# Performance work log

Measured on AMD Instinct MI355X. Metric: run time of the kernel, lower is better.

The kernel has to match this reference:

```python
import jax, jax.numpy as jnp
import numpy as np

L, N, E, F, D, ED, G = 3, 40000, 640000, 32, 64, 64, 16
EPS_LN = 1e-5
silu = jax.nn.silu


def graph_ln(x, gids, gamma, beta):
    # Per-graph LayerNorm: normalize over (nodes_in_graph, features), affine per feature.
    Dn = x.shape[1]
    cnt = jax.ops.segment_sum(jnp.ones((x.shape[0],), x.dtype), gids, num_segments=G) * Dn
    mean = jax.ops.segment_sum(x.sum(1), gids, num_segments=G) / cnt
    ex2 = jax.ops.segment_sum((x * x).sum(1), gids, num_segments=G) / cnt
    inv = jax.lax.rsqrt(ex2 - mean * mean + EPS_LN)
    return (x - mean[gids, None]) * inv[gids, None] * gamma + beta


def setup_inputs() -> dict:
    key = jax.random.key(0)
    it = iter(jax.random.split(key, 64))
    def rn(shape, s=0.1):
        return jax.random.normal(next(it), shape, jnp.float32) * s
    return {
        "node_features": jax.random.normal(next(it), (N, F), jnp.float32),
        "node_positions": jax.random.normal(next(it), (N, 3), jnp.float32) * 3.0,
        "edges": jax.random.randint(next(it), (E, 2), 0, N),
        "graph_ids": jnp.sort(jax.random.randint(next(it), (N,), 0, G)),
        "proj_W1": rn((F, F)), "proj_b1": jnp.zeros((F,), jnp.float32),
        "proj_W2": rn((F, D)), "proj_b2": jnp.zeros((D,), jnp.float32),
        "ef_W": rn((L, 1, ED)), "ef_b": jnp.zeros((L, ED), jnp.float32),
        "el_W1": rn((L, ED + 2 * D, 2 * D)), "el_b1": jnp.zeros((L, 2 * D), jnp.float32),
        "el_W2": rn((L, 2 * D, ED)), "el_b2": jnp.zeros((L, ED), jnp.float32),
        "in_W": rn((L, ED, 3 * D)), "in_b": jnp.zeros((L, 3 * D), jnp.float32),
        "msg_W1": rn((L, D, D)), "msg_b1": jnp.zeros((L, D), jnp.float32),
        "msg_W2": rn((L, D, 3 * D)), "msg_b2": jnp.zeros((L, 3 * D), jnp.float32),
        "ei_W": rn((L, D, 1)), "ei_b": jnp.zeros((L, 1), jnp.float32),
        "ln_g": jnp.ones((L, D), jnp.float32), "ln_b": jnp.zeros((L, D), jnp.float32),
        "up_UV": rn((L, D, 2 * D)),
        "uv_W1": rn((L, 2 * D, D)), "uv_b1": jnp.zeros((L, D), jnp.float32),
        "uv_W2": rn((L, D, 3 * D)), "uv_b2": jnp.zeros((L, 3 * D), jnp.float32),
    }


def _forward(node_features, node_positions, proj_W1, proj_b1, proj_W2, proj_b2,
             ef_W, ef_b, el_W1, el_b1, el_W2, el_b2, in_W, in_b,
             msg_W1, msg_b1, msg_W2, msg_b2, ei_W, ei_b, ln_g, ln_b,
             up_UV, uv_W1, uv_b1, uv_W2, uv_b2, edges, graph_ids):
    src, dst = edges[:, 0], edges[:, 1]
    diff = node_positions[dst] - node_positions[src]            # [E,3]
    dist = jnp.sqrt((diff * diff).sum(-1) + 1e-12)              # [E]
    unit = diff / dist[:, None]                                 # [E,3]
    edge_emb = dist[:, None]                                    # [E,1] (rbf_layer=None)
    s = silu(node_features @ proj_W1 + proj_b1) @ proj_W2 + proj_b2   # [N,D]
    v = jnp.zeros((s.shape[0], 3, D), s.dtype)                  # [N,3,D]
    for l in range(L):
        # edge featurizer
        es = silu(edge_emb @ ef_W[l] + ef_b[l])                 # [E,ED]
        # EdgeLayer (residual=False)
        cat = jnp.concatenate([s[src], s[dst], es], axis=1)     # [E,2D+ED]
        es = silu(cat @ el_W1[l] + el_b1[l]) @ el_W2[l] + el_b2[l]
        # InteractionLayer
        sn = graph_ln(s, graph_ids, ln_g[l], ln_b[l])
        Wv = es @ in_W[l] + in_b[l]                             # [E,3D]
        phi = silu(sn @ msg_W1[l] + msg_b1[l]) @ msg_W2[l] + msg_b2[l]  # [N,3D]
        Wphi = Wv * phi[src]
        phi_s, phi_vv, phi_vs = jnp.split(Wphi, 3, axis=1)
        gate = jax.nn.sigmoid(phi_s @ ei_W[l] + ei_b[l])        # [E,1]
        ms = phi_s * gate
        mv = (v[src] * phi_vv[:, None, :] + phi_vs[:, None, :] * unit[..., None]) * gate[:, None, :]
        s = sn + jax.ops.segment_sum(ms, dst, num_segments=N)
        v = v + jax.ops.segment_sum(mv, dst, num_segments=N)
        # UpdateLayer
        UVv = v @ up_UV[l]                                      # [N,3,2D]
        Uv, Vv = jnp.split(UVv, 2, axis=-1)
        Vv_norm = jnp.sqrt((Vv * Vv).sum(1) + 1e-6)             # [N,D]
        a = silu(jnp.concatenate([Vv_norm, s], axis=1) @ uv_W1[l] + uv_b1[l]) @ uv_W2[l] + uv_b2[l]
        a_vv, a_sv, a_ss = jnp.split(a, 3, axis=1)
        inner = (Uv * Vv).sum(1)                                # [N,D]
        s = s + a_ss + a_sv * inner
        v = v + a_vv[:, None, :] * Uv
    return s


def reference(node_features, node_positions, edges, graph_ids, proj_W1, proj_b1, proj_W2, proj_b2,
              ef_W, ef_b, el_W1, el_b1, el_W2, el_b2, in_W, in_b,
              msg_W1, msg_b1, msg_W2, msg_b2, ei_W, ei_b, ln_g, ln_b,
              up_UV, uv_W1, uv_b1, uv_W2, uv_b2):
    return _forward(node_features, node_positions, proj_W1, proj_b1, proj_W2, proj_b2,
                    ef_W, ef_b, el_W1, el_b1, el_W2, el_b2, in_W, in_b,
                    msg_W1, msg_b1, msg_W2, msg_b2, ei_W, ei_b, ln_g, ln_b,
                    up_UV, uv_W1, uv_b1, uv_W2, uv_b2, edges, graph_ids)
```

## Files before the change

kernel.cpp:

```cpp
#include <hip/hip_runtime.h>
#include <hip/hip_bf16.h>
#include <math.h>

#define NN 40000
#define EE 640000
#define GG 16
#define LL 3
#define TE 32

#define STC 200
#define STH 136
#define STE 72
#define PCAT (TE*STC)
#define PH1  (TE*STH)
#define PES  (TE*STE)
#define SWP_ST 196

typedef __attribute__((ext_vector_type(8))) short s8v;
typedef __attribute__((ext_vector_type(4))) float f4v;

__device__ __forceinline__ float silu_f(float x){ return x / (1.f + __expf(-x)); }
__device__ __forceinline__ float sigmoid_f(float x){ return 1.f / (1.f + __expf(-x)); }
__device__ __forceinline__ ushort f2b(float x){
  __hip_bfloat16 h = __float2bfloat16(x);
  return __builtin_bit_cast(ushort, h);
}
__device__ __forceinline__ float b2f(ushort u){
  uint x = ((uint)u) << 16;
  return __builtin_bit_cast(float, x);
}
__device__ __forceinline__ void split2(float v, ushort &hi, ushort &lo){
  uint b = __builtin_bit_cast(uint, v);
  hi = (ushort)(b >> 16);
  float rem = v - __builtin_bit_cast(float, b & 0xffff0000u);
  lo = (ushort)(__builtin_bit_cast(uint, rem) >> 16);
}

__global__ void k_geom(const float* __restrict__ pos, const int* __restrict__ edges,
                       float4* __restrict__ UD){
  int e = blockIdx.x*blockDim.x + threadIdx.x;
  if(e >= EE) return;
  int s = edges[2*e], d = edges[2*e+1];
  float dx = pos[3*d]-pos[3*s], dy = pos[3*d+1]-pos[3*s+1], dz = pos[3*d+2]-pos[3*s+2];
  float r = sqrtf(dx*dx+dy*dy+dz*dz + 1e-12f);
  float ir = 1.f/r;
  UD[e] = make_float4(dx*ir, dy*ir, dz*ir, r);
}

__global__ void k_counts(const int* __restrict__ gids, int* __restrict__ cnt){
  __shared__ int lb[GG+1];
  int g = threadIdx.x;
  if(g <= GG){
    int lo=0, hi=NN;
    while(lo<hi){ int m=(lo+hi)>>1; if(gids[m]<g) lo=m+1; else hi=m; }
    lb[g]=lo;
  }
  __syncthreads();
  if(g < GG) cnt[g] = lb[g+1]-lb[g];
}

__global__ void k_hist(const int* __restrict__ edges, int* __restrict__ HIST){
  int e = blockIdx.x*blockDim.x+threadIdx.x;
  if(e<EE) atomicAdd(&HIST[edges[2*e+1]], 1);
}

__global__ void k_scan(const int* __restrict__ HIST, int* __restrict__ BASE){
  __shared__ int ps[256];
  int t = threadIdx.x;
  const int CH = (NN+255)/256;
  int lo = t*CH, hi = lo+CH; if(hi>NN) hi=NN; if(lo>NN) lo=NN;
  int s=0;
  for(int i=lo;i<hi;i++) s += HIST[i];
  ps[t]=s;
  __syncthreads();
  if(t==0){ int run=0; for(int i=0;i<256;i++){ int v=ps[i]; ps[i]=run; run+=v; } }
  __syncthreads();
  int run = ps[t];
  for(int i=lo;i<hi;i++){ BASE[i]=run; run += HIST[i]; }
}

__global__ void k_scatter(const int* __restrict__ edges, const int* __restrict__ BASE,
                          int* __restrict__ CUR,
                          int* __restrict__ SRCp, int* __restrict__ DSTp,
                          const float4* __restrict__ UD, float4* __restrict__ UDP){
  int e = blockIdx.x*blockDim.x+threadIdx.x;
  if(e>=EE) return;
  int d = edges[2*e+1];
  int s = edges[2*e];
  int pos = BASE[d] + atomicAdd(&CUR[d], 1);
  SRCp[pos] = s;
  DSTp[pos] = d;
  UDP[pos]  = UD[e];
}

__global__ void k_prep_w(const float* __restrict__ elW1, const float* __restrict__ elW2,
                         const float* __restrict__ inW,
                         ushort* __restrict__ W1H, ushort* __restrict__ W1L,
                         ushort* __restrict__ W2H, ushort* __restrict__ W2L,
                         ushort* __restrict__ W3H, ushort* __restrict__ W3L){
  int tid = blockIdx.x*256 + threadIdx.x;
  const int per = 24576 + 8192 + 12288;
  if(tid >= LL*per) return;
  int l = tid/per, r = tid - l*per;
  float w; ushort* dh; ushort* dl; int idx;
  if(r < 24576){
    int n = r/192, k = r - n*192;
    w = elW1[l*24576 + k*128 + n];
    dh = W1H; dl = W1L; idx = l*24576 + r;
  } else if(r < 32768){
    int i = r - 24576; int n = i/128, k = i - n*128;
    w = elW2[l*8192 + k*64 + n];
    dh = W2H; dl = W2L; idx = l*8192 + i;
  } else {
    int i = r - 32768; int n = i/64, k = i - n*64;
    w = inW[l*12288 + k*192 + n];
    dh = W3H; dl = W3L; idx = l*12288 + i;
  }
  ushort hi = f2b(w);
  dh[idx] = hi;
  dl[idx] = f2b(w - b2f(hi));
}

__global__ void k_proj(const float* __restrict__ x,
                       const float* __restrict__ W1, const float* __restrict__ b1,
                       const float* __restrict__ W2, const float* __restrict__ b2,
                       float* __restrict__ S, ushort* __restrict__ SHL){
  int n = blockIdx.x*blockDim.x+threadIdx.x;
  if(n>=NN) return;
  float xr[32];
  #pragma unroll
  for(int k=0;k<32;k++) xr[k] = x[n*32+k];
  float h[32];
  #pragma unroll 4
  for(int j=0;j<32;j++){
    float a = b1[j];
    #pragma unroll
    for(int k=0;k<32;k++) a += xr[k]*W1[k*32+j];
    h[j] = silu_f(a);
  }
  #pragma unroll 4
  for(int d=0; d<64; d++){
    float a = b2[d];
    #pragma unroll
    for(int j=0;j<32;j++) a += h[j]*W2[j*64+d];
    S[n*64+d] = a;
    ushort hi = f2b(a);
    SHL[(size_t)n*128 + d] = hi;
    SHL[(size_t)n*128 + 64 + d] = f2b(a - b2f(hi));
  }
}

__global__ void k_ln_reduce(const float* __restrict__ S, const int* __restrict__ gids,
                            float* __restrict__ GS, float* __restrict__ GQ){
  __shared__ float ls[GG], lq[GG];
  int t = threadIdx.x;
  if(t<GG){ ls[t]=0.f; lq[t]=0.f; }
  __syncthreads();
  int n = blockIdx.x*blockDim.x+t;
  if(n<NN){
    const float4* p = reinterpret_cast<const float4*>(S + (size_t)n*64);
    float sm=0.f, sq=0.f;
    #pragma unroll
    for(int i=0;i<16;i++){ float4 v=p[i];
      sm += v.x+v.y+v.z+v.w;
      sq += v.x*v.x+v.y*v.y+v.z*v.z+v.w*v.w; }
    int g = gids[n];
    atomicAdd(&ls[g], sm); atomicAdd(&lq[g], sq);
  }
  __syncthreads();
  if(t<GG){ atomicAdd(&GS[t], ls[t]); atomicAdd(&GQ[t], lq[t]); }
}

__global__ void k_ln_final(const float* __restrict__ GS, const float* __restrict__ GQ,
                           const int* __restrict__ cnt,
                           float* __restrict__ MEANV, float* __restrict__ INVV){
  int g = threadIdx.x;
  if(g<GG){
    float c = (float)cnt[g]*64.f;
    float m = GS[g]/c, e2 = GQ[g]/c;
    MEANV[g]=m; INVV[g]=rsqrtf(e2 - m*m + 1e-5f);
  }
}

__global__ void k_node_pre(const float* __restrict__ S, const int* __restrict__ gids,
                           const float* __restrict__ MEANV, const float* __restrict__ INVV,
                           const float* __restrict__ lng, const float* __restrict__ lnb,
                           const float* __restrict__ W1, const float* __restrict__ b1,
                           const float* __restrict__ W2, const float* __restrict__ b2,
                           float* __restrict__ SN, ushort* __restrict__ PHI2){
  int t = threadIdx.x, w = t>>6, lane = t&63;
  int n = blockIdx.x*4 + w;
  __shared__ float sh[4][65];
  __shared__ float hh[4][65];
  if(n < NN){
    int g = gids[n];
    float snv = (S[(size_t)n*64+lane] - MEANV[g]) * INVV[g] * lng[lane] + lnb[lane];
    SN[(size_t)n*64+lane] = snv;
    sh[w][lane] = snv;
  }
  __syncthreads();
  if(n < NN){
    float a = b1[lane];
    #pragma unroll 8
    for(int k=0;k<64;k++) a += sh[w][k]*W1[k*64+lane];
    hh[w][lane] = silu_f(a);
  }
  __syncthreads();
  if(n < NN){
    #pragma unroll
    for(int m=0;m<3;m++){
      int j = lane + 64*m;
      float a = b2[j];
      #pragma unroll 8
      for(int k=0;k<64;k++) a += hh[w][k]*W2[k*192+j];
      ushort h_, l_; split2(a, h_, l_);
      PHI2[(size_t)n*384 + 2*j]     = h_;
      PHI2[(size_t)n*384 + 2*j + 1] = l_;
    }
  }
}

__global__ __launch_bounds__(256,3) void k_edge(
    const ushort* __restrict__ SHL, const ushort* __restrict__ PHI2,
    const ushort* __restrict__ V0b, const float4* __restrict__ UDP,
    const int* __restrict__ SRCp, const int* __restrict__ DSTp,
    const float* __restrict__ efW, const float* __restrict__ efb,
    const ushort* __restrict__ GW1H, const ushort* __restrict__ GW1L, const float* __restrict__ elb1,
    const ushort* __restrict__ GW2H, const ushort* __restrict__ GW2L, const float* __restrict__ elb2,
    const ushort* __restrict__ GW3H, const ushort* __restrict__ GW3L, const float* __restrict__ inb,
    const float* __restrict__ eiW, const float* __restrict__ eib,
    float* __restrict__ SN, float* __restrict__ V1, int hasV0)
{
  __shared__ __align__(16) ushort sCat[2*PCAT];
  __shared__ __align__(16) ushort sH1 [2*PH1];
  __shared__ __align__(16) ushort sEs [2*PES];
  __shared__ int   sSrc[TE], sDst[TE];
  __shared__ float sUnit[TE*3];
  __shared__ float sGate[TE];

  const int t  = threadIdx.x;
  const int cpx = gridDim.x >> 3;
  const int bid = (blockIdx.x & 7)*cpx + (blockIdx.x >> 3);
  const int p0 = bid * TE;
  const int w  = t >> 6, l = t & 63;
  const int lr = l & 15, lg = l >> 4;

  if(t < TE){
    int p = p0 + t;
    sSrc[t] = SRCp[p]; sDst[t] = DSTp[p];
    float4 ud = UDP[p];
    sUnit[3*t] = ud.x; sUnit[3*t+1] = ud.y; sUnit[3*t+2] = ud.z;
  }
  {
    int e = t >> 3, s = t & 7;
    int pg = p0 + e;
    int src = SRCp[pg], dst = DSTp[pg];
    float dist = UDP[pg].w;
    *reinterpret_cast<s8v*>(&sCat[e*STC + s*8]) =
        *reinterpret_cast<const s8v*>(&SHL[(size_t)src*128 + s*8]);
    *reinterpret_cast<s8v*>(&sCat[PCAT + e*STC + s*8]) =
        *reinterpret_cast<const s8v*>(&SHL[(size_t)src*128 + 64 + s*8]);
    *reinterpret_cast<s8v*>(&sCat[e*STC + 64 + s*8]) =
        *reinterpret_cast<const s8v*>(&SHL[(size_t)dst*128 + s*8]);
    *reinterpret_cast<s8v*>(&sCat[PCAT + e*STC + 64 + s*8]) =
        *reinterpret_cast<const s8v*>(&SHL[(size_t)dst*128 + 64 + s*8]);
    #pragma unroll
    for(int jj=0;jj<8;jj++){
      int j = s*8 + jj;
      float v = silu_f(dist*efW[j] + efb[j]);
      ushort h_, l_; split2(v, h_, l_);
      sCat[e*STC + 128 + j] = h_;
      sCat[PCAT + e*STC + 128 + j] = l_;
    }
  }
  __syncthreads();

  uint phu[2][3][4];
  #pragma unroll
  for(int rt=0; rt<2; rt++){
    #pragma unroll
    for(int r=0;r<4;r++){
      int srcp = sSrc[16*rt + lg*4 + r];
      #pragma unroll
      for(int jl=0;jl<3;jl++){
        int n = 16*(3*w+jl) + lr;
        phu[rt][jl][r] = *reinterpret_cast<const uint*>(&PHI2[(size_t)srcp*384 + 2*n]);
      }
    }
  }
  ushort v0pre[TE];
  if(w > 0 && hasV0){
    int c = w-1;
    #pragma unroll
    for(int p=0;p<TE;p++)
      v0pre[p] = V0b[(size_t)sSrc[p]*192 + c*64 + l];
  }

  #pragma unroll
  for(int jl=0;jl<2;jl++){
    s8v bh[6], bl[6];
    #pragma unroll
    for(int k=0;k<6;k++){
      int o = (16*(2*w+jl)+lr)*192 + k*32 + lg*8;
      bh[k] = *reinterpret_cast<const s8v*>(&GW1H[o]);
      bl[k] = *reinterpret_cast<const s8v*>(&GW1L[o]);
    }
    #pragma unroll
    for(int rt=0; rt<2; rt++){
      s8v ah[6], al[6];
      #pragma unroll
      for(int k=0;k<6;k++){
        int ro = (16*rt+lr)*STC + k*32 + lg*8;
        ah[k] = *reinterpret_cast<const s8v*>(&sCat[ro]);
        al[k] = *reinterpret_cast<const s8v*>(&sCat[PCAT + ro]);
      }
      float bv = elb1[16*(2*w+jl)+lr];
      f4v acc = (f4v){bv,bv,bv,bv};
      #pragma unroll
      for(int k=0;k<6;k++){
        acc = __builtin_amdgcn_mfma_f32_16x16x32_bf16(ah[k], bh[k], acc, 0,0,0);
        acc = __builtin_amdgcn_mfma_f32_16x16x32_bf16(al[k], bh[k], acc, 0,0,0);
        acc = __builtin_amdgcn_mfma_f32_16x16x32_bf16(ah[k], bl[k], acc, 0,0,0);
      }
      #pragma unroll
      for(int r=0;r<4;r++){
        float v = silu_f(acc[r]);
        ushort h_, l_; split2(v, h_, l_);
        int o = (16*rt + lg*4 + r)*STH + 16*(2*w+jl) + lr;
        sH1[o] = h_;
        sH1[PH1 + o] = l_;
      }
    }
  }
  __syncthreads();

  {
    s8v bh[4], bl[4];
    #pragma unroll
    for(int k=0;k<4;k++){
      int o = (16*w+lr)*128 + k*32 + lg*8;
      bh[k] = *reinterpret_cast<const s8v*>(&GW2H[o]);
      bl[k] = *reinterpret_cast<const s8v*>(&GW2L[o]);
    }
    #pragma unroll
    for(int rt=0; rt<2; rt++){
      s8v a2h[4], a2l[4];
      #pragma unroll
      for(int k=0;k<4;k++){
        int ro = (16*rt+lr)*STH + k*32 + lg*8;
        a2h[k] = *reinterpret_cast<const s8v*>(&sH1[ro]);
        a2l[k] = *reinterpret_cast<const s8v*>(&sH1[PH1 + ro]);
      }
      float bv = elb2[16*w + lr];
      f4v acc = (f4v){bv,bv,bv,bv};
      #pragma unroll
      for(int k=0;k<4;k++){
        acc = __builtin_amdgcn_mfma_f32_16x16x32_bf16(a2h[k], bh[k], acc, 0,0,0);
        acc = __builtin_amdgcn_mfma_f32_16x16x32_bf16(a2l[k], bh[k], acc, 0,0,0);
        acc = __builtin_amdgcn_mfma_f32_16x16x32_bf16(a2h[k], bl[k], acc, 0,0,0);
      }
      #pragma unroll
      for(int r=0;r<4;r++){
        ushort h_, l_; split2(acc[r], h_, l_);
        int o = (16*rt + lg*4 + r)*STE + 16*w + lr;
        sEs[o] = h_;
        sEs[PES + o] = l_;
      }
    }
  }
  __syncthreads();

  float* sWp = reinterpret_cast<float*>(sCat);
  #pragma unroll
  for(int jl=0;jl<3;jl++){
    const int n = 16*(3*w+jl) + lr;
    s8v bh[2], bl[2];
    #pragma unroll
    for(int k=0;k<2;k++){
      bh[k] = *reinterpret_cast<const s8v*>(&GW3H[n*64 + k*32 + lg*8]);
      bl[k] = *reinterpret_cast<const s8v*>(&GW3L[n*64 + k*32 + lg*8]);
    }
    #pragma unroll
    for(int rt=0; rt<2; rt++){
      s8v a3h[2], a3l[2];
      #pragma unroll
      for(int k=0;k<2;k++){
        int ro = (16*rt+lr)*STE + k*32 + lg*8;
        a3h[k] = *reinterpret_cast<const s8v*>(&sEs[ro]);
        a3l[k] = *reinterpret_cast<const s8v*>(&sEs[PES + ro]);
      }
      float bv = inb[n];
      f4v acc = (f4v){bv,bv,bv,bv};
      #pragma unroll
      for(int k=0;k<2;k++){
        acc = __builtin_amdgcn_mfma_f32_16x16x32_bf16(a3h[k], bh[k], acc, 0,0,0);
        acc = __builtin_amdgcn_mfma_f32_16x16x32_bf16(a3l[k], bh[k], acc, 0,0,0);
        acc = __builtin_amdgcn_mfma_f32_16x16x32_bf16(a3h[k], bl[k], acc, 0,0,0);
      }
      #pragma unroll
      for(int r=0;r<4;r++){
        uint u = phu[rt][jl][r];
        float phi = b2f((ushort)(u & 0xffffu)) + b2f((ushort)(u >> 16));
        sWp[(16*rt + lg*4 + r)*SWP_ST + n] = acc[r]*phi;
      }
    }
  }
  __syncthreads();

  float ei = eiW[l];
  #pragma unroll
  for(int i=0;i<8;i++){
    int e = w*8 + i;
    float gp = sWp[e*SWP_ST + l] * ei;
    #pragma unroll
    for(int off=1; off<64; off<<=1) gp += __shfl_xor(gp, off);
    if(l==0) sGate[e] = sigmoid_f(gp + eib[0]);
  }
  __syncthreads();

  if(w == 0){
    float acc = 0.f;
    #pragma unroll
    for(int p=0;p<TE;p++){
      acc += sWp[p*SWP_ST + l] * sGate[p];
      bool flush = (p==TE-1) || (sDst[p+1] != sDst[p]);
      if(flush){ atomicAdd(&SN[(size_t)sDst[p]*64 + l], acc); acc = 0.f; }
    }
  } else {
    int c = w-1;
    float acc = 0.f;
    #pragma unroll
    for(int p=0;p<TE;p++){
      float pvv = sWp[p*SWP_ST + 64 + l];
      float pvs = sWp[p*SWP_ST + 128 + l];
      float term = pvs*sUnit[p*3+c];
      if(hasV0) term += b2f(v0pre[p])*pvv;
      acc += term * sGate[p];
      bool flush = (p==TE-1) || (sDst[p+1] != sDst[p]);
      if(flush){ atomicAdd(&V1[(size_t)sDst[p]*192 + c*64 + l], acc); acc = 0.f; }
    }
  }
}

__global__ void k_node_post(const float* __restrict__ SN, const float* __restrict__ V1,
                            const float* __restrict__ upUV,
                            const float* __restrict__ uvW1, const float* __restrict__ uvb1,
                            const float* __restrict__ uvW2, const float* __restrict__ uvb2,
                            float* __restrict__ Sout, float* __restrict__ V0,
                            ushort* __restrict__ SHL, ushort* __restrict__ V0b)
{
  int t = threadIdx.x, w = t>>6, j = t&63;
  int n = blockIdx.x*4 + w;
  __shared__ float vsh[4][3][64];
  __shared__ float cat2[4][129];
  __shared__ float hh[4][65];
  if(n < NN){
    #pragma unroll
    for(int c=0;c<3;c++) vsh[w][c][j] = V1[(size_t)n*192 + c*64 + j];
  }
  __syncthreads();
  float Uv[3]={0,0,0}, Vv[3]={0,0,0};
  float s_new = 0.f;
  if(n < NN){
    #pragma unroll 4
    for(int k=0;k<64;k++){
      float wu = upUV[k*128 + j];
      float wv = upUV[k*128 + 64 + j];
      #pragma unroll
      for(int c=0;c<3;c++){ float vk = vsh[w][c][k]; Uv[c] += vk*wu; Vv[c] += vk*wv; }
    }
    s_new = SN[(size_t)n*64 + j];
    float vn2 = Vv[0]*Vv[0]+Vv[1]*Vv[1]+Vv[2]*Vv[2];
    cat2[w][j] = sqrtf(vn2 + 1e-6f);
    cat2[w][64+j] = s_new;
  }
  __syncthreads();
  if(n<NN){
    float a = uvb1[j];
    #pragma unroll 8
    for(int k=0;k<128;k++) a += cat2[w][k]*uvW1[k*64+j];
    hh[w][j] = silu_f(a);
  }
  __syncthreads();
  if(n<NN){
    float a0=uvb2[j], a1=uvb2[64+j], a2=uvb2[128+j];
    #pragma unroll 4
    for(int k=0;k<64;k++){
      float h = hh[w][k];
      a0 += h*uvW2[k*192+j]; a1 += h*uvW2[k*192+64+j]; a2 += h*uvW2[k*192+128+j];
    }
    float inner = Uv[0]*Vv[0]+Uv[1]*Vv[1]+Uv[2]*Vv[2];
    float sval = s_new + a2 + a1*inner;
    Sout[(size_t)n*64+j] = sval;
    ushort hi = f2b(sval);
    SHL[(size_t)n*128 + j] = hi;
    SHL[(size_t)n*128 + 64 + j] = f2b(sval - b2f(hi));
    #pragma unroll
    for(int c=0;c<3;c++){
      float vv = vsh[w][c][j] + a0*Uv[c];
      V0[(size_t)n*192 + c*64 + j] = vv;
      V0b[(size_t)n*192 + c*64 + j] = f2b(vv);
    }
  }
}

extern "C" void kernel_launch(void* const* d_in, const int* in_sizes, int n_in,
                              void* d_out, int out_size, void* d_ws, size_t ws_size,
                              hipStream_t stream)
{
  const float* node_features  = (const float*)d_in[0];
  const float* node_positions = (const float*)d_in[1];
  const int*   edges          = (const int*)  d_in[2];
  const int*   gids           = (const int*)  d_in[3];
  const float* proj_W1 = (const float*)d_in[4];
  const float* proj_b1 = (const float*)d_in[5];
  const float* proj_W2 = (const float*)d_in[6];
  const float* proj_b2 = (const float*)d_in[7];
  const float* ef_W  = (const float*)d_in[8];
  const float* ef_b  = (const float*)d_in[9];
  const float* el_W1 = (const float*)d_in[10];
  const float* el_b1 = (const float*)d_in[11];
  const float* el_W2 = (const float*)d_in[12];
  const float* el_b2 = (const float*)d_in[13];
  const float* in_W  = (const float*)d_in[14];
  const float* in_b  = (const float*)d_in[15];
  const float* msg_W1= (const float*)d_in[16];
  const float* msg_b1= (const float*)d_in[17];
  const float* msg_W2= (const float*)d_in[18];
  const float* msg_b2= (const float*)d_in[19];
  const float* ei_W  = (const float*)d_in[20];
  const float* ei_b  = (const float*)d_in[21];
  const float* ln_g  = (const float*)d_in[22];
  const float* ln_b  = (const float*)d_in[23];
  const float* up_UV = (const float*)d_in[24];
  const float* uv_W1 = (const float*)d_in[25];
  const float* uv_b1 = (const float*)d_in[26];
  const float* uv_W2 = (const float*)d_in[27];
  const float* uv_b2 = (const float*)d_in[28];

  float* ws = (float*)d_ws;
  size_t off = 0;
  float*  S    = ws + off; off += (size_t)NN*64;
  float*  SN   = ws + off; off += (size_t)NN*64;
  float*  V0   = ws + off; off += (size_t)NN*192;
  float*  V1   = ws + off; off += (size_t)NN*192;
  float4* UD   = (float4*)(ws + off); off += (size_t)EE*4;
  float4* UDP  = (float4*)(ws + off); off += (size_t)EE*4;
  float*  GS   = ws + off; off += GG;
  float*  GQ   = ws + off; off += GG;
  float*  MEANV= ws + off; off += GG;
  float*  INVV = ws + off; off += GG;
  int*    CNT  = (int*)(ws + off); off += GG;
  off = (off + 3) & ~(size_t)3;
  ushort* SHL  = (ushort*)(ws + off); off += (size_t)NN*64;
  ushort* PHI2 = (ushort*)(ws + off); off += (size_t)NN*192;
  ushort* V0b  = (ushort*)(ws + off); off += (size_t)NN*96;
  ushort* W1H = (ushort*)(ws + off); off += (size_t)LL*24576/2;
  ushort* W1L = (ushort*)(ws + off); off += (size_t)LL*24576/2;
  ushort* W2H = (ushort*)(ws + off); off += (size_t)LL*8192/2;
  ushort* W2L = (ushort*)(ws + off); off += (size_t)LL*8192/2;
  ushort* W3H = (ushort*)(ws + off); off += (size_t)LL*12288/2;
  ushort* W3L = (ushort*)(ws + off); off += (size_t)LL*12288/2;
  int*    HIST = (int*)(ws + off); off += NN;
  int*    BASE = (int*)(ws + off); off += NN;
  int*    CUR  = (int*)(ws + off); off += NN;
  int*    SRCp = (int*)(ws + off); off += EE;
  int*    DSTp = (int*)(ws + off); off += EE;

  hipMemsetAsync(HIST, 0, NN*sizeof(int), stream);
  hipMemsetAsync(CUR,  0, NN*sizeof(int), stream);
  hipMemsetAsync(V0, 0, (size_t)NN*192*sizeof(float), stream);
  hipMemsetAsync(V0b, 0, (size_t)NN*192*sizeof(ushort), stream);

  k_geom   <<<(EE+255)/256, 256, 0, stream>>>(node_positions, edges, UD);
  k_counts <<<1, 32, 0, stream>>>(gids, CNT);
  k_proj   <<<(NN+255)/256, 256, 0, stream>>>(node_features, proj_W1, proj_b1, proj_W2, proj_b2, S, SHL);
  k_prep_w <<<(LL*45056+255)/256, 256, 0, stream>>>(el_W1, el_W2, in_W,
                   W1H, W1L, W2H, W2L, W3H, W3L);
  k_hist   <<<(EE+255)/256, 256, 0, stream>>>(edges, HIST);
  k_scan   <<<1, 256, 0, stream>>>(HIST, BASE);
  k_scatter<<<(EE+255)/256, 256, 0, stream>>>(edges, BASE, CUR, SRCp, DSTp, UD, UDP);

  for(int l=0; l<LL; l++){
    hipMemsetAsync(GS, 0, 2*GG*sizeof(float), stream);
    k_ln_reduce<<<(NN+255)/256, 256, 0, stream>>>(S, gids, GS, GQ);
    k_ln_final <<<1, 64, 0, stream>>>(GS, GQ, CNT, MEANV, INVV);
    k_node_pre <<<(NN+3)/4, 256, 0, stream>>>(S, gids, MEANV, INVV,
                   ln_g + l*64, ln_b + l*64,
                   msg_W1 + l*64*64, msg_b1 + l*64,
                   msg_W2 + l*64*192, msg_b2 + l*192,
                   SN, PHI2);
    hipMemcpyAsync(V1, V0, (size_t)NN*192*sizeof(float), hipMemcpyDeviceToDevice, stream);
    k_edge<<<EE/TE, 256, 0, stream>>>(SHL, PHI2, V0b, UDP, SRCp, DSTp,
                   ef_W + l*64, ef_b + l*64,
                   W1H + l*24576, W1L + l*24576, el_b1 + l*128,
                   W2H + l*8192,  W2L + l*8192,  el_b2 + l*64,
                   W3H + l*12288, W3L + l*12288, in_b + l*192,
                   ei_W + l*64, ei_b + l, SN, V1, l > 0 ? 1 : 0);
    float* sout = (l == LL-1) ? (float*)d_out : S;
    k_node_post<<<(NN+3)/4, 256, 0, stream>>>(SN, V1,
                   up_UV + l*64*128,
                   uv_W1 + l*128*64, uv_b1 + l*64,
                   uv_W2 + l*64*192, uv_b2 + l*192, sout, V0, SHL, V0b);
  }
}
```

Measured before the change: 2.419 ms.

## Fuse graph-LN statistics into producer kernels and update V in place

Per-graph LayerNorm sum and sum-of-squares are now accumulated inside k_proj and k_node_post, with wavefront shuffles and shared atomics, so the separate k_ln_reduce pass and the per-layer memset are gone. k_ln_final resets the accumulators for the next layer. The V0 buffer and the device-to-device copy into V1 are removed by having k_node_post write the updated vector features back into V1 in place. k_node_pre's dot products use two accumulators for more ILP. Together these cut several extra passes over node data per layer, at the cost of more global atomics and an in-place update that relies on each node being read and written only by its own wavefront.

```diff
diff --git a/kernel.cpp b/kernel.cpp
--- a/kernel.cpp
+++ b/kernel.cpp
@@ -121,57 +121,48 @@
   dl[idx] = f2b(w - b2f(hi));
 }
 
-__global__ void k_proj(const float* __restrict__ x,
+__global__ void k_proj(const float* __restrict__ x, const int* __restrict__ gids,
                        const float* __restrict__ W1, const float* __restrict__ b1,
                        const float* __restrict__ W2, const float* __restrict__ b2,
-                       float* __restrict__ S, ushort* __restrict__ SHL){
-  int n = blockIdx.x*blockDim.x+threadIdx.x;
-  if(n>=NN) return;
-  float xr[32];
-  #pragma unroll
-  for(int k=0;k<32;k++) xr[k] = x[n*32+k];
-  float h[32];
-  #pragma unroll 4
-  for(int j=0;j<32;j++){
-    float a = b1[j];
-    #pragma unroll
-    for(int k=0;k<32;k++) a += xr[k]*W1[k*32+j];
-    h[j] = silu_f(a);
-  }
-  #pragma unroll 4
-  for(int d=0; d<64; d++){
-    float a = b2[d];
-    #pragma unroll
-    for(int j=0;j<32;j++) a += h[j]*W2[j*64+d];
-    S[n*64+d] = a;
-    ushort hi = f2b(a);
-    SHL[(size_t)n*128 + d] = hi;
-    SHL[(size_t)n*128 + 64 + d] = f2b(a - b2f(hi));
-  }
-}
-
-__global__ void k_ln_reduce(const float* __restrict__ S, const int* __restrict__ gids,
-                            float* __restrict__ GS, float* __restrict__ GQ){
+                       float* __restrict__ S, ushort* __restrict__ SHL,
+                       float* __restrict__ GS, float* __restrict__ GQ){
   __shared__ float ls[GG], lq[GG];
   int t = threadIdx.x;
-  if(t<GG){ ls[t]=0.f; lq[t]=0.f; }
-  __syncthreads();
-  int n = blockIdx.x*blockDim.x+t;
-  if(n<NN){
-    const float4* p = reinterpret_cast<const float4*>(S + (size_t)n*64);
+  if(t < GG){ ls[t]=0.f; lq[t]=0.f; }
+  __syncthreads();
+  int n = blockIdx.x*blockDim.x + t;
+  if(n < NN){
+    float xr[32];
+    #pragma unroll
+    for(int k=0;k<32;k++) xr[k] = x[n*32+k];
+    float h[32];
+    #pragma unroll 4
+    for(int j=0;j<32;j++){
+      float a = b1[j];
+      #pragma unroll
+      for(int k=0;k<32;k++) a += xr[k]*W1[k*32+j];
+      h[j] = silu_f(a);
+    }
     float sm=0.f, sq=0.f;
-    #pragma unroll
-    for(int i=0;i<16;i++){ float4 v=p[i];
-      sm += v.x+v.y+v.z+v.w;
-      sq += v.x*v.x+v.y*v.y+v.z*v.z+v.w*v.w; }
+    #pragma unroll 4
+    for(int d=0; d<64; d++){
+      float a = b2[d];
+      #pragma unroll
+      for(int j=0;j<32;j++) a += h[j]*W2[j*64+d];
+      S[n*64+d] = a;
+      sm += a; sq += a*a;
+      ushort hi = f2b(a);
+      SHL[(size_t)n*128 + d] = hi;
+      SHL[(size_t)n*128 + 64 + d] = f2b(a - b2f(hi));
+    }
     int g = gids[n];
     atomicAdd(&ls[g], sm); atomicAdd(&lq[g], sq);
   }
   __syncthreads();
-  if(t<GG){ atomicAdd(&GS[t], ls[t]); atomicAdd(&GQ[t], lq[t]); }
-}
-
-__global__ void k_ln_final(const float* __restrict__ GS, const float* __restrict__ GQ,
+  if(t < GG){ atomicAdd(&GS[t], ls[t]); atomicAdd(&GQ[t], lq[t]); }
+}
+
+__global__ void k_ln_final(float* __restrict__ GS, float* __restrict__ GQ,
                            const int* __restrict__ cnt,
                            float* __restrict__ MEANV, float* __restrict__ INVV){
   int g = threadIdx.x;
@@ -179,6 +170,7 @@
     float c = (float)cnt[g]*64.f;
     float m = GS[g]/c, e2 = GQ[g]/c;
     MEANV[g]=m; INVV[g]=rsqrtf(e2 - m*m + 1e-5f);
+    GS[g]=0.f; GQ[g]=0.f;
   }
 }
 
@@ -200,19 +192,26 @@
   }
   __syncthreads();
   if(n < NN){
-    float a = b1[lane];
+    float a0 = b1[lane], a1 = 0.f;
     #pragma unroll 8
-    for(int k=0;k<64;k++) a += sh[w][k]*W1[k*64+lane];
-    hh[w][lane] = silu_f(a);
+    for(int k=0;k<64;k+=2){
+      a0 += sh[w][k]*W1[k*64+lane];
+      a1 += sh[w][k+1]*W1[(k+1)*64+lane];
+    }
+    hh[w][lane] = silu_f(a0+a1);
   }
   __syncthreads();
   if(n < NN){
     #pragma unroll
     for(int m=0;m<3;m++){
       int j = lane + 64*m;
-      float a = b2[j];
+      float a0 = b2[j], a1 = 0.f;
       #pragma unroll 8
-      for(int k=0;k<64;k++) a += hh[w][k]*W2[k*192+j];
+      for(int k=0;k<64;k+=2){
+        a0 += hh[w][k]*W2[k*192+j];
+        a1 += hh[w][k+1]*W2[(k+1)*192+j];
+      }
+      float a = a0+a1;
       ushort h_, l_; split2(a, h_, l_);
       PHI2[(size_t)n*384 + 2*j]     = h_;
       PHI2[(size_t)n*384 + 2*j + 1] = l_;
@@ -442,18 +441,22 @@
   }
 }
 
-__global__ void k_node_post(const float* __restrict__ SN, const float* __restrict__ V1,
+__global__ void k_node_post(const float* __restrict__ SN, float* __restrict__ V1,
                             const float* __restrict__ upUV,
                             const float* __restrict__ uvW1, const float* __restrict__ uvb1,
                             const float* __restrict__ uvW2, const float* __restrict__ uvb2,
-                            float* __restrict__ Sout, float* __restrict__ V0,
-                            ushort* __restrict__ SHL, ushort* __restrict__ V0b)
+                            float* __restrict__ Sout,
+                            ushort* __restrict__ SHL, ushort* __restrict__ V0b,
+                            const int* __restrict__ gids,
+                            float* __restrict__ GS, float* __restrict__ GQ)
 {
   int t = threadIdx.x, w = t>>6, j = t&63;
   int n = blockIdx.x*4 + w;
   __shared__ float vsh[4][3][64];
   __shared__ float cat2[4][129];
   __shared__ float hh[4][65];
+  __shared__ float lsS[GG], lsQ[GG];
+  if(t < GG){ lsS[t]=0.f; lsQ[t]=0.f; }
   if(n < NN){
     #pragma unroll
     for(int c=0;c<3;c++) vsh[w][c][j] = V1[(size_t)n*192 + c*64 + j];
@@ -498,10 +501,22 @@
     #pragma unroll
     for(int c=0;c<3;c++){
       float vv = vsh[w][c][j] + a0*Uv[c];
-      V0[(size_t)n*192 + c*64 + j] = vv;
+      V1[(size_t)n*192 + c*64 + j] = vv;
       V0b[(size_t)n*192 + c*64 + j] = f2b(vv);
     }
-  }
+    float sm = sval, sq = sval*sval;
+    #pragma unroll
+    for(int off=1; off<64; off<<=1){
+      sm += __shfl_xor(sm, off);
+      sq += __shfl_xor(sq, off);
+    }
+    if(j == 0){
+      int g = gids[n];
+      atomicAdd(&lsS[g], sm); atomicAdd(&lsQ[g], sq);
+    }
+  }
+  __syncthreads();
+  if(t < GG){ atomicAdd(&GS[t], lsS[t]); atomicAdd(&GQ[t], lsQ[t]); }
 }
 
 extern "C" void kernel_launch(void* const* d_in, const int* in_sizes, int n_in,
@@ -542,7 +557,6 @@
   size_t off = 0;
   float*  S    = ws + off; off += (size_t)NN*64;
   float*  SN   = ws + off; off += (size_t)NN*64;
-  float*  V0   = ws + off; off += (size_t)NN*192;
   float*  V1   = ws + off; off += (size_t)NN*192;
   float4* UD   = (float4*)(ws + off); off += (size_t)EE*4;
   float4* UDP  = (float4*)(ws + off); off += (size_t)EE*4;
@@ -569,12 +583,13 @@
 
   hipMemsetAsync(HIST, 0, NN*sizeof(int), stream);
   hipMemsetAsync(CUR,  0, NN*sizeof(int), stream);
-  hipMemsetAsync(V0, 0, (size_t)NN*192*sizeof(float), stream);
+  hipMemsetAsync(V1, 0, (size_t)NN*192*sizeof(float), stream);
   hipMemsetAsync(V0b, 0, (size_t)NN*192*sizeof(ushort), stream);
+  hipMemsetAsync(GS, 0, 2*GG*sizeof(float), stream);
 
   k_geom   <<<(EE+255)/256, 256, 0, stream>>>(node_positions, edges, UD);
   k_counts <<<1, 32, 0, stream>>>(gids, CNT);
-  k_proj   <<<(NN+255)/256, 256, 0, stream>>>(node_features, proj_W1, proj_b1, proj_W2, proj_b2, S, SHL);
+  k_proj   <<<(NN+255)/256, 256, 0, stream>>>(node_features, gids, proj_W1, proj_b1, proj_W2, proj_b2, S, SHL, GS, GQ);
   k_prep_w <<<(LL*45056+255)/256, 256, 0, stream>>>(el_W1, el_W2, in_W,
                    W1H, W1L, W2H, W2L, W3H, W3L);
   k_hist   <<<(EE+255)/256, 256, 0, stream>>>(edges, HIST);
@@ -582,15 +597,12 @@
   k_scatter<<<(EE+255)/256, 256, 0, stream>>>(edges, BASE, CUR, SRCp, DSTp, UD, UDP);
 
   for(int l=0; l<LL; l++){
-    hipMemsetAsync(GS, 0, 2*GG*sizeof(float), stream);
-    k_ln_reduce<<<(NN+255)/256, 256, 0, stream>>>(S, gids, GS, GQ);
     k_ln_final <<<1, 64, 0, stream>>>(GS, GQ, CNT, MEANV, INVV);
     k_node_pre <<<(NN+3)/4, 256, 0, stream>>>(S, gids, MEANV, INVV,
                    ln_g + l*64, ln_b + l*64,
                    msg_W1 + l*64*64, msg_b1 + l*64,
                    msg_W2 + l*64*192, msg_b2 + l*192,
                    SN, PHI2);
-    hipMemcpyAsync(V1, V0, (size_t)NN*192*sizeof(float), hipMemcpyDeviceToDevice, stream);
     k_edge<<<EE/TE, 256, 0, stream>>>(SHL, PHI2, V0b, UDP, SRCp, DSTp,
                    ef_W + l*64, ef_b + l*64,
                    W1H + l*24576, W1L + l*24576, el_b1 + l*128,
@@ -601,6 +613,7 @@
     k_node_post<<<(NN+3)/4, 256, 0, stream>>>(SN, V1,
                    up_UV + l*64*128,
                    uv_W1 + l*128*64, uv_b1 + l*64,
-                   uv_W2 + l*64*192, uv_b2 + l*192, sout, V0, SHL, V0b);
-  }
-}
+                   uv_W2 + l*64*192, uv_b2 + l*192, sout, SHL, V0b,
+                   gids, GS, GQ);
+  }
+}
```

Result: no change. 2.448 ms (+1.2%).
